# Optimization experiments

Hardware: AMD Instinct MI355X
Metric: run time of the kernel (lower is better)

Reference implementation:

```python
import jax, jax.numpy as jnp
import numpy as np

KH = KW = 3
DH = DW = 1

def _extract_patches(x, kh, kw, dh, dw):
    # x: [B, C, H, W] -> patches: [B, C, OH, OW, kh*kw] matching torch unfold order
    B, C, H, W = x.shape
    oh = (H - kh) // dh + 1
    ow = (W - kw) // dw + 1
    cols = []
    for i in range(kh):
        for j in range(kw):
            cols.append(x[:, :, i:i + oh * dh:dh, j:j + ow * dw:dw])
    return jnp.stack(cols, axis=-1)  # [B, C, OH, OW, k*k]


def setup_inputs() -> dict:
    key = jax.random.key(0)
    k1, k2 = jax.random.split(key)
    x = jax.random.normal(k1, (64, 32, 64, 64), dtype=jnp.float32)
    weight = jax.random.normal(k2, (1, 64, 32, 62, 62, 9), dtype=jnp.float32)
    return {"x": x, "weight": weight}


def reference(x, weight):
    # patches: [B, Cin, OH, OW, K2]; weight[0]: [Cout, Cin, OH, OW, K2]
    patches = _extract_patches(x, KH, KW, DH, DW)
    # per-location dot product over (Cin, K2) -> [B, Cout, OH, OW]
    out = jnp.einsum('bihwk,oihwk->bohw', patches, weight[0])
    return out
```

## Files before the change

kernel.cpp:

```cpp
#include <hip/hip_runtime.h>


#define OWDIM 62
#define LOCS 3844
#define WSI 34596u
#define XM 131072u

__device__ __forceinline__ float f4get(const float4 v, int j) {
    return j == 0 ? v.x : j == 1 ? v.y : j == 2 ? v.z : v.w;
}
__device__ __forceinline__ void fma4(float4& a, float s, const float4 x) {
    a.x = fmaf(s, x.x, a.x);
    a.y = fmaf(s, x.y, a.y);
    a.z = fmaf(s, x.z, a.z);
    a.w = fmaf(s, x.w, a.w);
}

__global__ void lc2d_transpose_x(const float* __restrict__ x, float* __restrict__ xT) {
    __shared__ float tile[64][65];
    const int m0 = blockIdx.x * 64;
    const int t = threadIdx.x;
    const int c = t & 63, q = t >> 6;
#pragma unroll
    for (int jj = 0; jj < 16; ++jj) {
        const int b = q * 16 + jj;
        tile[c][b] = x[(size_t)b * XM + (size_t)(m0 + c)];
    }
    __syncthreads();
#pragma unroll
    for (int jj = 0; jj < 16; ++jj) {
        const int m = q * 16 + jj;
        xT[(size_t)(m0 + m) * 64u + (size_t)c] = tile[m][c];
    }
}

__global__ __launch_bounds__(256, 2) void lc2d_main(const float* __restrict__ w,
                                                    const float* __restrict__ xT,
                                                    float* __restrict__ out) {
    __shared__ float Wl[4][2][9][64];

    const int bid = blockIdx.x;
    const int t = (bid & 7) * 124 + (bid >> 3);
    const int ohalf = (t >= 496) ? 1 : 0;
    const int rem = t - ohalf * 496;
    const int oh = rem >> 3;
    const int t8 = rem & 7;
    const int ow0 = (t8 < 7) ? (t8 << 3) : 54;
    const int loc0 = oh * OWDIM + ow0;

    const int lane = threadIdx.x & 63;
    const int wave = __builtin_amdgcn_readfirstlane((int)(threadIdx.x >> 6));
    const int bg = lane & 7;
    const int og = lane >> 3;
    const int o_base = ohalf * 32 + wave * 8;

    const float* wsrc = w + (size_t)(o_base + og) * 32u * WSI + (size_t)(loc0 + bg) * 9u;

    float4 accA[8], accB[8];
#pragma unroll
    for (int l = 0; l < 8; ++l) {
        accA[l] = make_float4(0.f, 0.f, 0.f, 0.f);
        accB[l] = make_float4(0.f, 0.f, 0.f, 0.f);
    }

#pragma unroll
    for (int f = 0; f < 9; ++f)
        __builtin_amdgcn_global_load_lds(
            (const __attribute__((address_space(1))) unsigned int*)(wsrc + f),
            (__attribute__((address_space(3))) unsigned int*)&Wl[wave][0][f][0], 4, 0, 0);

#pragma unroll 1
    for (int i = 0; i < 32; ++i) {
        const int buf = i & 1;

        asm volatile("s_waitcnt vmcnt(0)" ::: "memory");
        __builtin_amdgcn_sched_barrier(0);

        if (i < 31) {
            const float* s = wsrc + (size_t)(i + 1) * WSI;
#pragma unroll
            for (int f = 0; f < 9; ++f)
                __builtin_amdgcn_global_load_lds(
                    (const __attribute__((address_space(1))) unsigned int*)(s + f),
                    (__attribute__((address_space(3))) unsigned int*)&Wl[wave][buf ^ 1][f][0], 4, 0, 0);
        }
        __builtin_amdgcn_sched_barrier(0);

        const float* wl = &Wl[wave][buf][0][0];
#pragma unroll
        for (int r = 0; r < 3; ++r) {
            float4 wqa[3], wqb[3];
#pragma unroll
            for (int cc = 0; cc < 3; ++cc) {
                wqa[cc] = *(const float4*)(wl + (r * 3 + cc) * 64 + og * 8);
                wqb[cc] = *(const float4*)(wl + (r * 3 + cc) * 64 + og * 8 + 4);
            }
            const float* xb = xT + ((size_t)i * 4096u + (size_t)((oh + r) * 64 + ow0)) * 64u
                                 + (size_t)(bg * 8);
            float4 Xa[10], Xb[10];
#pragma unroll
            for (int m = 0; m < 10; ++m) {
                Xa[m] = *(const float4*)(xb + (size_t)(m * 64));
                Xb[m] = *(const float4*)(xb + (size_t)(m * 64) + 4);
            }
#pragma unroll
            for (int m = 0; m < 10; ++m) {
#pragma unroll
                for (int cc = 0; cc < 3; ++cc) {
                    const int l = m - cc;
                    if (l >= 0 && l < 8) {
                        const float ws = (l < 4) ? f4get(wqa[cc], l & 3) : f4get(wqb[cc], l & 3);
                        fma4(accA[l], ws, Xa[m]);
                        fma4(accB[l], ws, Xb[m]);
                    }
                }
            }
        }
    }

    const int o = o_base + og;
#define ACCV(db, l) ((db) < 4 ? f4get(accA[(l)], (db)) : f4get(accB[(l)], (db) - 4))
#pragma unroll
    for (int db = 0; db < 8; ++db) {
        float* po = out + (size_t)((bg * 8 + db) * 64 + o) * (size_t)LOCS + (size_t)loc0;
        *(float2*)(po + 0) = make_float2(ACCV(db, 0), ACCV(db, 1));
        *(float2*)(po + 2) = make_float2(ACCV(db, 2), ACCV(db, 3));
        *(float2*)(po + 4) = make_float2(ACCV(db, 4), ACCV(db, 5));
        *(float2*)(po + 6) = make_float2(ACCV(db, 6), ACCV(db, 7));
    }
#undef ACCV
}

extern "C" void kernel_launch(void* const* d_in, const int* in_sizes, int n_in,
                              void* d_out, int out_size, void* d_ws, size_t ws_size,
                              hipStream_t stream) {
    const float* x = (const float*)d_in[0];
    const float* w = (const float*)d_in[1];
    float* out = (float*)d_out;
    float* xT = (float*)d_ws;

    lc2d_transpose_x<<<dim3(XM / 64), dim3(256), 0, stream>>>(x, xT);
    lc2d_main<<<dim3(992), dim3(256), 0, stream>>>(w, xT, out);
}
```

Before: 399.4 us.

## Load weights directly into registers and remap threads to 16 batch groups

Drops the LDS double-buffered weight staging through global_load_lds. Each thread now loads its 72 contiguous weight floats for one output channel straight into registers as float4 vectors. Threads are remapped to 16 batch groups of 4 and 4 output channels per wave, which halves the per-thread accumulators. The grid doubles to 1984 blocks and launch bounds ask for 3 blocks per SM to raise occupancy. In exchange, x data is reused less per thread, and weight loads are now exposed with no explicit prefetch.

```diff
diff --git a/kernel.cpp b/kernel.cpp
--- a/kernel.cpp
+++ b/kernel.cpp
@@ -34,101 +34,68 @@
     }
 }
 
-__global__ __launch_bounds__(256, 2) void lc2d_main(const float* __restrict__ w,
+#define WGET(l, k) f4get(W[((l) * 9 + (k)) >> 2], ((l) * 9 + (k)) & 3)
+
+__global__ __launch_bounds__(256, 3) void lc2d_main(const float* __restrict__ w,
                                                     const float* __restrict__ xT,
                                                     float* __restrict__ out) {
-    __shared__ float Wl[4][2][9][64];
-
     const int bid = blockIdx.x;
-    const int t = (bid & 7) * 124 + (bid >> 3);
-    const int ohalf = (t >= 496) ? 1 : 0;
-    const int rem = t - ohalf * 496;
-    const int oh = rem >> 3;
-    const int t8 = rem & 7;
+    const int t = (bid & 7) * 248 + (bid >> 3);
+    const int oq = t & 3;
+    const int rest = t >> 2;
+    const int oh = rest >> 3;
+    const int t8 = rest & 7;
     const int ow0 = (t8 < 7) ? (t8 << 3) : 54;
     const int loc0 = oh * OWDIM + ow0;
 
     const int lane = threadIdx.x & 63;
     const int wave = __builtin_amdgcn_readfirstlane((int)(threadIdx.x >> 6));
-    const int bg = lane & 7;
-    const int og = lane >> 3;
-    const int o_base = ohalf * 32 + wave * 8;
+    const int bg = lane & 15;
+    const int og = lane >> 4;
+    const int o = oq * 16 + wave * 4 + og;
 
-    const float* wsrc = w + (size_t)(o_base + og) * 32u * WSI + (size_t)(loc0 + bg) * 9u;
+    const float* wbase = w + (size_t)((o * 32) * (size_t)LOCS + loc0) * 9u;
+    const float* xbase = xT + (size_t)(bg * 4);
 
-    float4 accA[8], accB[8];
+    float4 acc[8];
 #pragma unroll
-    for (int l = 0; l < 8; ++l) {
-        accA[l] = make_float4(0.f, 0.f, 0.f, 0.f);
-        accB[l] = make_float4(0.f, 0.f, 0.f, 0.f);
-    }
-
-#pragma unroll
-    for (int f = 0; f < 9; ++f)
-        __builtin_amdgcn_global_load_lds(
-            (const __attribute__((address_space(1))) unsigned int*)(wsrc + f),
-            (__attribute__((address_space(3))) unsigned int*)&Wl[wave][0][f][0], 4, 0, 0);
+    for (int l = 0; l < 8; ++l) acc[l] = make_float4(0.f, 0.f, 0.f, 0.f);
 
 #pragma unroll 1
     for (int i = 0; i < 32; ++i) {
-        const int buf = i & 1;
+        const float* wr = wbase + (size_t)i * WSI;
+        float4 W[18];
+#pragma unroll
+        for (int j = 0; j < 18; ++j) W[j] = *(const float4*)(wr + 4 * j);
 
-        asm volatile("s_waitcnt vmcnt(0)" ::: "memory");
-        __builtin_amdgcn_sched_barrier(0);
-
-        if (i < 31) {
-            const float* s = wsrc + (size_t)(i + 1) * WSI;
-#pragma unroll
-            for (int f = 0; f < 9; ++f)
-                __builtin_amdgcn_global_load_lds(
-                    (const __attribute__((address_space(1))) unsigned int*)(s + f),
-                    (__attribute__((address_space(3))) unsigned int*)&Wl[wave][buf ^ 1][f][0], 4, 0, 0);
-        }
-        __builtin_amdgcn_sched_barrier(0);
-
-        const float* wl = &Wl[wave][buf][0][0];
 #pragma unroll
         for (int r = 0; r < 3; ++r) {
-            float4 wqa[3], wqb[3];
+            const float* xp = xbase + ((size_t)i * 4096u + (size_t)((oh + r) * 64 + ow0)) * 64u;
+            float4 Xa[10];
 #pragma unroll
-            for (int cc = 0; cc < 3; ++cc) {
-                wqa[cc] = *(const float4*)(wl + (r * 3 + cc) * 64 + og * 8);
-                wqb[cc] = *(const float4*)(wl + (r * 3 + cc) * 64 + og * 8 + 4);
-            }
-            const float* xb = xT + ((size_t)i * 4096u + (size_t)((oh + r) * 64 + ow0)) * 64u
-                                 + (size_t)(bg * 8);
-            float4 Xa[10], Xb[10];
-#pragma unroll
-            for (int m = 0; m < 10; ++m) {
-                Xa[m] = *(const float4*)(xb + (size_t)(m * 64));
-                Xb[m] = *(const float4*)(xb + (size_t)(m * 64) + 4);
-            }
+            for (int m = 0; m < 10; ++m)
+                Xa[m] = *(const float4*)(xp + (size_t)(m * 64));
 #pragma unroll
             for (int m = 0; m < 10; ++m) {
 #pragma unroll
                 for (int cc = 0; cc < 3; ++cc) {
                     const int l = m - cc;
-                    if (l >= 0 && l < 8) {
-                        const float ws = (l < 4) ? f4get(wqa[cc], l & 3) : f4get(wqb[cc], l & 3);
-                        fma4(accA[l], ws, Xa[m]);
-                        fma4(accB[l], ws, Xb[m]);
-                    }
+                    if (l >= 0 && l < 8)
+                        fma4(acc[l], WGET(l, r * 3 + cc), Xa[m]);
                 }
             }
+            __builtin_amdgcn_sched_barrier(0);
         }
     }
 
-    const int o = o_base + og;
-#define ACCV(db, l) ((db) < 4 ? f4get(accA[(l)], (db)) : f4get(accB[(l)], (db) - 4))
 #pragma unroll
-    for (int db = 0; db < 8; ++db) {
-        float* po = out + (size_t)((bg * 8 + db) * 64 + o) * (size_t)LOCS + (size_t)loc0;
-        *(float2*)(po + 0) = make_float2(ACCV(db, 0), ACCV(db, 1));
-        *(float2*)(po + 2) = make_float2(ACCV(db, 2), ACCV(db, 3));
-        *(float2*)(po + 4) = make_float2(ACCV(db, 4), ACCV(db, 5));
-        *(float2*)(po + 6) = make_float2(ACCV(db, 6), ACCV(db, 7));
+    for (int db = 0; db < 4; ++db) {
+        float* po = out + (size_t)((bg * 4 + db) * 64 + o) * (size_t)LOCS + (size_t)loc0;
+        *(float2*)(po + 0) = make_float2(f4get(acc[0], db), f4get(acc[1], db));
+        *(float2*)(po + 2) = make_float2(f4get(acc[2], db), f4get(acc[3], db));
+        *(float2*)(po + 4) = make_float2(f4get(acc[4], db), f4get(acc[5], db));
+        *(float2*)(po + 6) = make_float2(f4get(acc[6], db), f4get(acc[7], db));
     }
-#undef ACCV
 }
 
 extern "C" void kernel_launch(void* const* d_in, const int* in_sizes, int n_in,
@@ -140,5 +107,5 @@
     float* xT = (float*)d_ws;
 
     lc2d_transpose_x<<<dim3(XM / 64), dim3(256), 0, stream>>>(x, xT);
-    lc2d_main<<<dim3(992), dim3(256), 0, stream>>>(w, xT, out);
+    lc2d_main<<<dim3(1984), dim3(256), 0, stream>>>(w, xT, out);
 }
```

Result: slower. 1.264 ms (+216.5%).
